# Performance work log

Measured on AMD Instinct MI355X. Metric: run time of the kernel, lower is better.

The kernel has to match this reference:

```python
import jax, jax.numpy as jnp
import numpy as np

BLOCK = 128
FP8_MAX = 448.0  # max representable value of float8_e4m3fn
F8 = jnp.float8_e4m3fn


def setup_inputs() -> dict:
    key = jax.random.key(0)
    k1, k2, k3 = jax.random.split(key, 3)
    M, K, N = 4096, 7168, 16384
    x = jax.random.normal(k1, (M, K), jnp.float32)
    w = jax.random.normal(k2, (N, K), jnp.float32)  # raw weight; cast to fp8 in reference to simulate stored fp8
    w_scale = jax.random.uniform(k3, (N // BLOCK, K // BLOCK), jnp.float32, 0.5, 1.5)
    return {"x": x, "w": w, "w_scale": w_scale, "block_size": BLOCK}


def act_quant(x, b):
    M, K = x.shape
    xb = x.reshape(M, K // b, b)
    s = jnp.max(jnp.abs(xb), axis=-1) / FP8_MAX  # [M, K//b]
    xq = (xb / s[..., None]).astype(F8).astype(jnp.float32).reshape(M, K)
    return xq, s


def reference(x, w, w_scale, block_size):
    b = block_size
    # simulate fp8-stored weight (element_size == 1 branch)
    w8 = w.astype(F8).astype(jnp.float32)  # [N, K]
    # fp8_gemm: y[m,n] = sum_k xq[m,k]*w8[n,k]*xs[m,kb]*ws[nb,kb]
    # scales factor per-element, so dequantize both operands then one dense GEMM
    xq, xs = act_quant(x, b)
    x_dq = xq * jnp.repeat(xs, b, axis=1)                         # [M, K]
    w_dq = w8 * jnp.repeat(jnp.repeat(w_scale, b, axis=0), b, axis=1)  # [N, K]
    return x_dq @ w_dq.T  # [M, N], no bias (bias=False)
```

## Files before the change

### kernel.cpp

```cpp
#include <hip/hip_runtime.h>
#include <hip/hip_bf16.h>
#include <hip/hip_fp8.h>

typedef __attribute__((ext_vector_type(4))) float f32x4;
typedef __attribute__((ext_vector_type(2))) long long ll2;

#define AS1 __attribute__((address_space(1)))
#define AS3 __attribute__((address_space(3)))

static constexpr int Mdim = 4096;
static constexpr int Kdim = 7168;
static constexpr int Ndim = 16384;
static constexpr int KB   = Kdim / 128;
static constexpr float FP8_MAX = 448.0f;

#define BARRIER() do { asm volatile("" ::: "memory"); \
                       __builtin_amdgcn_s_barrier();  \
                       asm volatile("" ::: "memory"); } while (0)

#define MFMA_FP8 __builtin_amdgcn_mfma_f32_16x16x32_fp8_fp8

__global__ __launch_bounds__(256) void quant_x_kernel(
    const float* __restrict__ x, unsigned char* __restrict__ xq,
    float* __restrict__ xst)
{
    constexpr int NBLK = Mdim * KB;
    const int lane = threadIdx.x & 63;
    const int wid  = (blockIdx.x * 256 + threadIdx.x) >> 6;
    const int nw   = (gridDim.x * 256) >> 6;

    for (int b = wid; b < NBLK; b += nw) {
        size_t base = (size_t)b * 128 + lane * 2;
        float2 v = *reinterpret_cast<const float2*>(x + base);
        float amax = fmaxf(fabsf(v.x), fabsf(v.y));
#pragma unroll
        for (int off = 32; off > 0; off >>= 1)
            amax = fmaxf(amax, __shfl_xor(amax, off));
        float s = amax * (1.0f / FP8_MAX);
        unsigned char q0 = 0, q1 = 0;
        if (s > 0.0f) {
            q0 = __hip_fp8_e4m3(v.x / s).__x;
            q1 = __hip_fp8_e4m3(v.y / s).__x;
        }
        *reinterpret_cast<unsigned short*>(xq + base) =
            (unsigned short)(q0 | ((unsigned short)q1 << 8));
        if (lane == 0) {
            int row = b / KB, kb = b - row * KB;
            xst[(size_t)kb * Mdim + row] = s;
        }
    }
}

__global__ __launch_bounds__(256) void quant_w_kernel(
    const float* __restrict__ w, unsigned char* __restrict__ w8)
{
    constexpr size_t NCHUNK = (size_t)Ndim * Kdim / 8;

    size_t idx    = (size_t)blockIdx.x * 256 + threadIdx.x;
    size_t stride = (size_t)gridDim.x * 256;

    for (size_t c = idx; c < NCHUNK; c += stride) {
        const float* src = w + c * 8;
        float4 v0 = *reinterpret_cast<const float4*>(src);
        float4 v1 = *reinterpret_cast<const float4*>(src + 4);
        unsigned int lo = (unsigned int)__hip_fp8_e4m3(v0.x).__x
                        | ((unsigned int)__hip_fp8_e4m3(v0.y).__x << 8)
                        | ((unsigned int)__hip_fp8_e4m3(v0.z).__x << 16)
                        | ((unsigned int)__hip_fp8_e4m3(v0.w).__x << 24);
        unsigned int hi = (unsigned int)__hip_fp8_e4m3(v1.x).__x
                        | ((unsigned int)__hip_fp8_e4m3(v1.y).__x << 8)
                        | ((unsigned int)__hip_fp8_e4m3(v1.z).__x << 16)
                        | ((unsigned int)__hip_fp8_e4m3(v1.w).__x << 24);
        uint2 p; p.x = lo; p.y = hi;
        *reinterpret_cast<uint2*>(w8 + c * 8) = p;
    }
}

constexpr int BM = 256, BN = 128, BK = 64;
constexpr int NT  = Kdim / BK;
constexpr int NBN = Ndim / BN;
constexpr int NWG = (Mdim / BM) * NBN;
constexpr int K1  = Kdim;
constexpr int BUFSZ  = 24576;
constexpr int XS_OFF = 49152;
constexpr int WS_OFF = XS_OFF + 56 * 1024;
constexpr int LDS_TOT = WS_OFF + 224;

__global__ __launch_bounds__(512, 2) void gemm_fp8_kernel(
    const unsigned char* __restrict__ Ag,
    const unsigned char* __restrict__ Bg,
    const float* __restrict__ xsT,
    const float* __restrict__ Wsc,
    float* __restrict__ C)
{
    extern __shared__ char smem[];

    const int tid  = threadIdx.x;
    const int w    = tid >> 6;
    const int lane = tid & 63;
    const int wr   = w >> 1;
    const int wc   = w & 1;
    const int lr   = lane & 15;
    const int lk   = lane >> 4;

    int bid = (int)blockIdx.x;
    int swz = (bid & 7) * (NWG >> 3) + (bid >> 3);
    const int bm = (swz / NBN) * BM;
    const int bn = (swz % NBN) * BN;

    const int colF = (lk ^ ((lr >> 1) & 3)) << 4;
    const int aRow = wr * 64;
    const int bRow = wc * 64;

    const char* xsL0 = smem + XS_OFF + (wr * 64 + lk * 4) * 4;
    const char* wsL  = smem + WS_OFF;

    const int rowS = tid >> 2;
    const int colS = (((tid & 3) ^ ((rowS >> 1) & 3))) * 16;
    const size_t offG = (size_t)rowS * K1 + colS;
    const int ldsW = w * 1024;

    const char* Ab = (const char*)Ag + (size_t)bm * K1;
    const char* Bb = (const char*)Bg + (size_t)bn * K1;

    auto stage = [&](int T, int r) {
        if (T >= NT) return;
        const int regByte = (T & 1) * BUFSZ + r * 8192;
        const char* g = (r == 2 ? Bb : Ab + (size_t)r * (128 * (size_t)K1))
                        + (size_t)T * 64 + offG;
        __builtin_amdgcn_global_load_lds((const AS1 void*)g,
                                         (AS3 void*)(smem + regByte + ldsW),
                                         16, 0, 0);
    };

#pragma unroll
    for (int i = 0; i < 7; ++i) {
        const int kb = i * 8 + w;
        const float* g = xsT + (size_t)kb * Mdim + bm + lane * 4;
        __builtin_amdgcn_global_load_lds((const AS1 void*)g,
            (AS3 void*)(smem + XS_OFF + i * 8192 + ldsW), 16, 0, 0);
    }
    if (w == 0 && lane < 14) {
        const float* g = Wsc + (size_t)(bn >> 7) * KB + lane * 4;
        __builtin_amdgcn_global_load_lds((const AS1 void*)g,
            (AS3 void*)(smem + WS_OFF), 16, 0, 0);
    }
    stage(0, 0); stage(0, 1); stage(0, 2);
    stage(1, 2);
    asm volatile("s_waitcnt vmcnt(1)" ::: "memory");
    BARRIER();

    f32x4 acc[4][4] = {};

    for (int t = 0; t < NT; ++t) {
        const int buf = t & 1;
        const int kb  = t >> 1;
        const char* aB = smem + buf * BUFSZ;
        const char* bB = smem + buf * BUFSZ + 16384;
        ll2 a[4], b0[2], b1[2];
        f32x4 sv[4];

        const float wsv  = *(const float*)(wsL + kb * 4);
        const char* xsLk = xsL0 + (kb << 10);

        stage(t + 1, 0);
        stage(t + 1, 1);
#pragma unroll
        for (int m = 0; m < 4; ++m)
            a[m] = *(const ll2*)(aB + (aRow + m * 16 + lr) * 64 + colF);
#pragma unroll
        for (int n = 0; n < 2; ++n)
            b0[n] = *(const ll2*)(bB + (bRow + n * 16 + lr) * 64 + colF);
#pragma unroll
        for (int n = 0; n < 2; ++n)
            b1[n] = *(const ll2*)(bB + (bRow + (n + 2) * 16 + lr) * 64 + colF);
#pragma unroll
        for (int m = 0; m < 4; ++m)
            sv[m] = *reinterpret_cast<const f32x4*>(xsLk + m * 64) * wsv;
        __builtin_amdgcn_s_setprio(1);
#pragma unroll
        for (int m = 0; m < 4; ++m)
#pragma unroll
            for (int n = 0; n < 2; ++n) {
                f32x4 pacc = {0.f, 0.f, 0.f, 0.f};
                pacc = MFMA_FP8(a[m][0], b0[n][0], pacc, 0, 0, 0);
                pacc = MFMA_FP8(a[m][1], b0[n][1], pacc, 0, 0, 0);
                acc[m][n] += sv[m] * pacc;
            }
        __builtin_amdgcn_s_setprio(0);
        asm volatile("s_waitcnt lgkmcnt(0)" ::: "memory");
        BARRIER();

        stage(t + 2, 2);
        __builtin_amdgcn_s_setprio(1);
#pragma unroll
        for (int m = 0; m < 4; ++m)
#pragma unroll
            for (int n = 0; n < 2; ++n) {
                f32x4 pacc = {0.f, 0.f, 0.f, 0.f};
                pacc = MFMA_FP8(a[m][0], b1[n][0], pacc, 0, 0, 0);
                pacc = MFMA_FP8(a[m][1], b1[n][1], pacc, 0, 0, 0);
                acc[m][n + 2] += sv[m] * pacc;
            }
        __builtin_amdgcn_s_setprio(0);
        if (t < NT - 2) { asm volatile("s_waitcnt vmcnt(1)" ::: "memory"); }
        else            { asm volatile("s_waitcnt vmcnt(0)" ::: "memory"); }
        BARRIER();
    }

#pragma unroll
    for (int m = 0; m < 4; ++m) {
#pragma unroll
        for (int n = 0; n < 4; ++n) {
            const int row0 = bm + wr * 64 + m * 16 + lk * 4;
            const int col  = bn + wc * 64 + n * 16 + lr;
#pragma unroll
            for (int j = 0; j < 4; ++j)
                C[(size_t)(row0 + j) * Ndim + col] = acc[m][n][j];
        }
    }
}

extern "C" void kernel_launch(void* const* d_in, const int* in_sizes, int n_in,
                              void* d_out, int out_size, void* d_ws, size_t ws_size,
                              hipStream_t stream) {
    const float* x  = (const float*)d_in[0];
    const float* w  = (const float*)d_in[1];
    const float* ws = (const float*)d_in[2];

    unsigned char* xq  = (unsigned char*)d_ws;
    unsigned char* w8  = xq + (size_t)Mdim * Kdim;
    float*         xst = (float*)(w8 + (size_t)Ndim * Kdim);

    quant_x_kernel<<<2048, 256, 0, stream>>>(x, xq, xst);
    quant_w_kernel<<<4096, 256, 0, stream>>>(w, w8);

    hipFuncSetAttribute((const void*)gemm_fp8_kernel,
                        hipFuncAttributeMaxDynamicSharedMemorySize, LDS_TOT);
    gemm_fp8_kernel<<<NWG, 512, LDS_TOT, stream>>>(xq, w8, xst, ws,
                                                   (float*)d_out);
}
```

Before: 1.082 ms.

## Split GEMM workgroup across 16 waves with 64x32 per-wave tiles

Raises the GEMM workgroup from 512 to 1024 threads, arranged as a 4x4 wave grid, so each wave computes a 64x32 output tile instead of 64x64. Staging of A is spread over all 16 waves, B over the first 8, and the activation-scale preload is redistributed to match. Scale vectors are now reloaded only on even K-steps. The aim is more waves in flight to hide LDS and global latency. The cost is less register-level reuse of A fragments per MFMA, more LDS traffic per flop, and heavier barriers across 16 waves. With launch bounds of 4 and about 106KB of LDS per block, only one workgroup fits per CU.

```diff
diff --git a/kernel.cpp b/kernel.cpp
--- a/kernel.cpp
+++ b/kernel.cpp
@@ -86,7 +86,7 @@
 constexpr int WS_OFF = XS_OFF + 56 * 1024;
 constexpr int LDS_TOT = WS_OFF + 224;
 
-__global__ __launch_bounds__(512, 2) void gemm_fp8_kernel(
+__global__ __launch_bounds__(1024, 4) void gemm_fp8_kernel(
     const unsigned char* __restrict__ Ag,
     const unsigned char* __restrict__ Bg,
     const float* __restrict__ xsT,
@@ -98,8 +98,8 @@
     const int tid  = threadIdx.x;
     const int w    = tid >> 6;
     const int lane = tid & 63;
-    const int wr   = w >> 1;
-    const int wc   = w & 1;
+    const int wr   = w >> 2;
+    const int wc   = w & 3;
     const int lr   = lane & 15;
     const int lk   = lane >> 4;
 
@@ -110,7 +110,7 @@
 
     const int colF = (lk ^ ((lr >> 1) & 3)) << 4;
     const int aRow = wr * 64;
-    const int bRow = wc * 64;
+    const int bRow = wc * 32;
 
     const char* xsL0 = smem + XS_OFF + (wr * 64 + lk * 4) * 4;
     const char* wsL  = smem + WS_OFF;
@@ -123,97 +123,101 @@
     const char* Ab = (const char*)Ag + (size_t)bm * K1;
     const char* Bb = (const char*)Bg + (size_t)bn * K1;
 
-    auto stage = [&](int T, int r) {
+    auto stageA = [&](int T) {
         if (T >= NT) return;
-        const int regByte = (T & 1) * BUFSZ + r * 8192;
-        const char* g = (r == 2 ? Bb : Ab + (size_t)r * (128 * (size_t)K1))
-                        + (size_t)T * 64 + offG;
+        const char* g = Ab + (size_t)T * 64 + offG;
         __builtin_amdgcn_global_load_lds((const AS1 void*)g,
-                                         (AS3 void*)(smem + regByte + ldsW),
-                                         16, 0, 0);
+            (AS3 void*)(smem + (T & 1) * BUFSZ + ldsW), 16, 0, 0);
     };
-
-#pragma unroll
-    for (int i = 0; i < 7; ++i) {
-        const int kb = i * 8 + w;
-        const float* g = xsT + (size_t)kb * Mdim + bm + lane * 4;
+    auto stageB = [&](int T) {
+        if (T >= NT) return;
+        const char* g = Bb + (size_t)T * 64 + offG;
         __builtin_amdgcn_global_load_lds((const AS1 void*)g,
-            (AS3 void*)(smem + XS_OFF + i * 8192 + ldsW), 16, 0, 0);
+            (AS3 void*)(smem + (T & 1) * BUFSZ + 16384 + ldsW), 16, 0, 0);
+    };
+
+#pragma unroll
+    for (int i = 0; i < 4; ++i) {
+        const int c = i * 1024 + tid;
+        if (i < 3 || w < 8) {
+            const int kb  = c >> 6;
+            const int row = (c & 63) * 4;
+            const float* g = xsT + (size_t)kb * Mdim + bm + row;
+            __builtin_amdgcn_global_load_lds((const AS1 void*)g,
+                (AS3 void*)(smem + XS_OFF + i * 16384 + ldsW), 16, 0, 0);
+        }
     }
     if (w == 0 && lane < 14) {
         const float* g = Wsc + (size_t)(bn >> 7) * KB + lane * 4;
         __builtin_amdgcn_global_load_lds((const AS1 void*)g,
             (AS3 void*)(smem + WS_OFF), 16, 0, 0);
     }
-    stage(0, 0); stage(0, 1); stage(0, 2);
-    stage(1, 2);
-    asm volatile("s_waitcnt vmcnt(1)" ::: "memory");
+    stageA(0);
+    if (w < 8) { stageB(0); stageB(1); }
+    if (w < 8) { asm volatile("s_waitcnt vmcnt(1)" ::: "memory"); }
+    else       { asm volatile("s_waitcnt vmcnt(0)" ::: "memory"); }
     BARRIER();
 
-    f32x4 acc[4][4] = {};
+    f32x4 acc[4][2] = {};
+    f32x4 sv[4];
 
     for (int t = 0; t < NT; ++t) {
         const int buf = t & 1;
-        const int kb  = t >> 1;
         const char* aB = smem + buf * BUFSZ;
         const char* bB = smem + buf * BUFSZ + 16384;
-        ll2 a[4], b0[2], b1[2];
-        f32x4 sv[4];
-
-        const float wsv  = *(const float*)(wsL + kb * 4);
-        const char* xsLk = xsL0 + (kb << 10);
-
-        stage(t + 1, 0);
-        stage(t + 1, 1);
+        ll2 a[4], b0, b1;
+
+        stageA(t + 1);
 #pragma unroll
         for (int m = 0; m < 4; ++m)
             a[m] = *(const ll2*)(aB + (aRow + m * 16 + lr) * 64 + colF);
-#pragma unroll
-        for (int n = 0; n < 2; ++n)
-            b0[n] = *(const ll2*)(bB + (bRow + n * 16 + lr) * 64 + colF);
-#pragma unroll
-        for (int n = 0; n < 2; ++n)
-            b1[n] = *(const ll2*)(bB + (bRow + (n + 2) * 16 + lr) * 64 + colF);
-#pragma unroll
-        for (int m = 0; m < 4; ++m)
-            sv[m] = *reinterpret_cast<const f32x4*>(xsLk + m * 64) * wsv;
+        b0 = *(const ll2*)(bB + (bRow + lr) * 64 + colF);
+        b1 = *(const ll2*)(bB + (bRow + 16 + lr) * 64 + colF);
+        if (!(t & 1)) {
+            const int kb = t >> 1;
+            const float wsv  = *(const float*)(wsL + kb * 4);
+            const char* xsLk = xsL0 + (kb << 10);
+#pragma unroll
+            for (int m = 0; m < 4; ++m)
+                sv[m] = *reinterpret_cast<const f32x4*>(xsLk + m * 64) * wsv;
+        }
         __builtin_amdgcn_s_setprio(1);
 #pragma unroll
-        for (int m = 0; m < 4; ++m)
-#pragma unroll
-            for (int n = 0; n < 2; ++n) {
-                f32x4 pacc = {0.f, 0.f, 0.f, 0.f};
-                pacc = MFMA_FP8(a[m][0], b0[n][0], pacc, 0, 0, 0);
-                pacc = MFMA_FP8(a[m][1], b0[n][1], pacc, 0, 0, 0);
-                acc[m][n] += sv[m] * pacc;
-            }
+        for (int m = 0; m < 4; ++m) {
+            f32x4 pacc = {0.f, 0.f, 0.f, 0.f};
+            pacc = MFMA_FP8(a[m][0], b0[0], pacc, 0, 0, 0);
+            pacc = MFMA_FP8(a[m][1], b0[1], pacc, 0, 0, 0);
+            acc[m][0] += sv[m] * pacc;
+        }
         __builtin_amdgcn_s_setprio(0);
         asm volatile("s_waitcnt lgkmcnt(0)" ::: "memory");
         BARRIER();
 
-        stage(t + 2, 2);
+        if (w < 8) stageB(t + 2);
         __builtin_amdgcn_s_setprio(1);
 #pragma unroll
-        for (int m = 0; m < 4; ++m)
-#pragma unroll
-            for (int n = 0; n < 2; ++n) {
-                f32x4 pacc = {0.f, 0.f, 0.f, 0.f};
-                pacc = MFMA_FP8(a[m][0], b1[n][0], pacc, 0, 0, 0);
-                pacc = MFMA_FP8(a[m][1], b1[n][1], pacc, 0, 0, 0);
-                acc[m][n + 2] += sv[m] * pacc;
-            }
+        for (int m = 0; m < 4; ++m) {
+            f32x4 pacc = {0.f, 0.f, 0.f, 0.f};
+            pacc = MFMA_FP8(a[m][0], b1[0], pacc, 0, 0, 0);
+            pacc = MFMA_FP8(a[m][1], b1[1], pacc, 0, 0, 0);
+            acc[m][1] += sv[m] * pacc;
+        }
         __builtin_amdgcn_s_setprio(0);
-        if (t < NT - 2) { asm volatile("s_waitcnt vmcnt(1)" ::: "memory"); }
-        else            { asm volatile("s_waitcnt vmcnt(0)" ::: "memory"); }
+        if (t < NT - 2) {
+            if (w < 8) { asm volatile("s_waitcnt vmcnt(1)" ::: "memory"); }
+            else       { asm volatile("s_waitcnt vmcnt(0)" ::: "memory"); }
+        } else {
+            asm volatile("s_waitcnt vmcnt(0)" ::: "memory");
+        }
         BARRIER();
     }
 
 #pragma unroll
     for (int m = 0; m < 4; ++m) {
 #pragma unroll
-        for (int n = 0; n < 4; ++n) {
+        for (int n = 0; n < 2; ++n) {
             const int row0 = bm + wr * 64 + m * 16 + lk * 4;
-            const int col  = bn + wc * 64 + n * 16 + lr;
+            const int col  = bn + wc * 32 + n * 16 + lr;
 #pragma unroll
             for (int j = 0; j < 4; ++j)
                 C[(size_t)(row0 + j) * Ndim + col] = acc[m][n][j];
@@ -237,6 +241,6 @@
 
     hipFuncSetAttribute((const void*)gemm_fp8_kernel,
                         hipFuncAttributeMaxDynamicSharedMemorySize, LDS_TOT);
-    gemm_fp8_kernel<<<NWG, 512, LDS_TOT, stream>>>(xq, w8, xst, ws,
-                                                   (float*)d_out);
-}
+    gemm_fp8_kernel<<<NWG, 1024, LDS_TOT, stream>>>(xq, w8, xst, ws,
+                                                    (float*)d_out);
+}
```

Measured after the change: 1.008 ms. 6.8% less time.
